# Kernel tuning notes

Measured on AMD Instinct MI355X. Metric: run time of the kernel, lower is better.

## Reference

```python
import jax, jax.numpy as jnp
import numpy as np

R_MIN = 0.01
R_MAX = 0.6
H = 32            # polar radial bins (after pooling)
W = 64            # polar angular bins (after pooling)
UP_R = 10         # radial upsampling factor
UP_T = 10         # angular upsampling factor
ATT_ALPHA = 5.0
B, C, IMG = 64, 3, 224


def _conv(x, w, b):
    # NCHW valid conv, stride 1 (matches nn.Conv2d default padding=0)
    y = jax.lax.conv_general_dilated(x, w, (1, 1), 'VALID',
                                     dimension_numbers=('NCHW', 'OIHW', 'NCHW'))
    return y + b[None, :, None, None]


def _maxpool2(x):
    return jax.lax.reduce_window(x, -jnp.inf, jax.lax.max,
                                 (1, 1, 2, 2), (1, 1, 2, 2), 'VALID')


def _grid_sample_border(x, grid):
    # F.grid_sample, bilinear, padding_mode='border', align_corners=False
    Bn, Cn, Hi, Wi = x.shape
    ix = ((grid[..., 0] + 1.0) * Wi - 1.0) * 0.5   # x-coord -> width index
    iy = ((grid[..., 1] + 1.0) * Hi - 1.0) * 0.5   # y-coord -> height index
    x0f = jnp.floor(ix)
    y0f = jnp.floor(iy)
    wx = (ix - x0f)[..., None]
    wy = (iy - y0f)[..., None]
    x0 = jnp.clip(x0f.astype(jnp.int32), 0, Wi - 1)
    x1 = jnp.clip(x0f.astype(jnp.int32) + 1, 0, Wi - 1)
    y0 = jnp.clip(y0f.astype(jnp.int32), 0, Hi - 1)
    y1 = jnp.clip(y0f.astype(jnp.int32) + 1, 0, Hi - 1)
    bidx = jnp.arange(Bn)[:, None, None]
    v00 = x[bidx, :, y0, x0]   # [B,Hg,Wg,C]
    v01 = x[bidx, :, y0, x1]
    v10 = x[bidx, :, y1, x0]
    v11 = x[bidx, :, y1, x1]
    out = (v00 * (1 - wx) * (1 - wy) + v01 * wx * (1 - wy)
           + v10 * (1 - wx) * wy + v11 * wx * wy)
    return jnp.transpose(out, (0, 3, 1, 2))  # [B,C,Hg,Wg]


def setup_inputs() -> dict:
    key = jax.random.key(0)
    ks = jax.random.split(key, 10)
    x = jax.random.normal(ks[0], (B, C, IMG, IMG), dtype=jnp.float32)
    l_t_prev = jax.random.uniform(ks[1], (B, 2), dtype=jnp.float32)
    conv1_w = jax.random.normal(ks[2], (6, C, 5, 5), dtype=jnp.float32) * 0.1
    conv1_b = jnp.zeros((6,), jnp.float32)
    conv2_w = jax.random.normal(ks[3], (16, 6, 5, 5), dtype=jnp.float32) * 0.1
    conv2_b = jnp.zeros((16,), jnp.float32)
    fc1_w = jax.random.normal(ks[4], (8, 16), dtype=jnp.float32) * 0.1
    fc1_b = jnp.zeros((8,), jnp.float32)
    fc2_w = jax.random.normal(ks[5], (2, 8), dtype=jnp.float32) * 0.1
    fc2_b = jnp.zeros((2,), jnp.float32)
    return dict(x=x, l_t_prev=l_t_prev, conv1_w=conv1_w, conv1_b=conv1_b,
                conv2_w=conv2_w, conv2_b=conv2_b, fc1_w=fc1_w, fc1_b=fc1_b,
                fc2_w=fc2_w, fc2_b=fc2_b)


def reference(x, l_t_prev, conv1_w, conv1_b, conv2_w, conv2_b,
              fc1_w, fc1_b, fc2_w, fc2_b):
    # --- attention branch: conv -> maxpool -> conv -> GAP -> fc -> sigmoid ---
    h = _conv(x, conv1_w, conv1_b)
    h = _maxpool2(h)
    h = _conv(h, conv2_w, conv2_b)
    feat = h.mean(axis=(2, 3))                     # AdaptiveAvgPool2d(1), [B,16]
    h = jax.nn.relu(feat @ fc1_w.T + fc1_b)
    weight = jax.nn.sigmoid(h @ fc2_w.T + fc2_b) * ATT_ALPHA   # [B,2]
    # --- per-batch log-polar grid ---
    Hg, Wg = H * UP_R, W * UP_T
    angle = 2.0 * jnp.pi * jnp.arange(Wg, dtype=jnp.float32) / Wg
    unit = jnp.stack([jnp.sin(angle), jnp.cos(angle)], axis=-1)   # [Wg,2]
    start = jnp.log(R_MIN * weight[:, 0])
    stop = jnp.log(R_MAX * weight[:, 1])
    t = jnp.arange(Hg, dtype=jnp.float32) / (Hg - 1)
    radii = jnp.exp(start[:, None] + (stop - start)[:, None] * t[None])  # [B,Hg]
    grid = radii[:, :, None, None] * unit[None, None]     # [B,Hg,Wg,2]
    grid = grid + l_t_prev[:, None, None, :]
    # --- irregular bilinear sampling + box filter ---
    sampled = _grid_sample_border(x, grid)                 # [B,C,Hg,Wg]
    Bn, Cn = sampled.shape[:2]
    pooled = sampled.reshape(Bn, Cn, H, UP_R, W, UP_T).mean(axis=(3, 5))
    return pooled, weight
```

## Files before the change

### kernel.cpp

```cpp
#include <hip/hip_runtime.h>
#include <math.h>

#define Bn    64
#define Cn    3
#define IMG   224
#define PLANE (IMG*IMG)
#define C1    6
#define P1    110
#define P2    106
#define NVALID (P2*P2)
#define Hh    32
#define Ww    64
#define UPR   10
#define UPT   10
#define Hg    (Hh*UPR)
#define Wg    (Ww*UPT)
#define POOLED_SIZE (Bn*Cn*Hh*Ww)
#define NCHUNK 28
#define PSTRIDE 152
#define ROWB  (IMG*8)
#define TPB1  448

typedef unsigned short u16;
typedef unsigned long long ull;
typedef _Float16 h8v __attribute__((ext_vector_type(8)));
typedef float f4v __attribute__((ext_vector_type(4)));

#define PART_FLOATS ((size_t)Bn * NCHUNK * PSTRIDE)
#define X4B_U16     ((size_t)Bn * PLANE * 4)
#define WS_NEEDED   ((PART_FLOATS + Bn * 2) * 4 + X4B_U16 * 2)

__device__ __forceinline__ unsigned hpack(float a, float b) {
    union { _Float16 h; u16 u; } x, y;
    x.h = (_Float16)a; y.h = (_Float16)b;
    return (unsigned)x.u | ((unsigned)y.u << 16);
}
__device__ __forceinline__ float h2lo(unsigned v) {
    union { _Float16 h; u16 u; } c; c.u = (u16)(v & 0xffffu); return (float)c.h;
}
__device__ __forceinline__ float h2hi(unsigned v) {
    union { _Float16 h; u16 u; } c; c.u = (u16)(v >> 16); return (float)c.h;
}

#define GSHFL(v, idx) __shfl((v), (lane & 48) + (idx), 64)

__device__ __forceinline__ void conv_chunk(
    const unsigned char* xs, const h8v* a, f4v binit,
    int wid, int lane, int n, int g, int tid, int chunk,
    float (*rowR)[C1][4], float (*edgeLo)[C1][4], float (*edgeHi)[C1][4],
    float* __restrict__ partial_slot)
{
    float colsum[4][4];
    #pragma unroll
    for (int py = 0; py < 4; ++py)
        #pragma unroll
        for (int e = 0; e < 4; ++e) colsum[py][e] = 0.0f;

    #pragma unroll
    for (int si = 0; si < 2; ++si) {
        const int s = wid * 2 + si;
        const unsigned sByte = (unsigned)(s * 128 + n * 8 + g * 16);

        f4v acc[8];
        #pragma unroll
        for (int q = 0; q < 8; ++q) acc[q] = binit;

        #pragma unroll
        for (int r = 0; r < 12; ++r) {
            h8v bf;
            const unsigned char* bp = xs + r * ROWB + sByte;
            ((ull*)&bf)[0] = *(const ull*)bp;
            ((ull*)&bf)[1] = *(const ull*)(bp + 8);
            #pragma unroll
            for (int ky = 0; ky < 5; ++ky) {
                const int q = r - ky;
                if (q >= 0 && q < 8)
                    acc[q] = __builtin_amdgcn_mfma_f32_16x16x32_f16(
                        a[ky], bf, acc[q], 0, 0, 0);
            }
        }

        #pragma unroll
        for (int py = 0; py < 4; ++py) {
            #pragma unroll
            for (int e = 0; e < 4; ++e) {
                float t = fmaxf(acc[2 * py][e], acc[2 * py + 1][e]);
                t = fmaxf(t, __shfl_xor(t, 1, 64));
                if (s == 13 && n >= 12) t = 0.0f;
                colsum[py][e] += t;
                const int oc = g * 4 + e;
                if (s == 0) {
                    const float c0 = GSHFL(t, 0), c1 = GSHFL(t, 2);
                    const float c2 = GSHFL(t, 4), c3 = GSHFL(t, 6);
                    const float S1 = c0, S2 = S1 + c1, S3 = S2 + c2, S4 = S3 + c3;
                    const float sv = (n == 0) ? S1 : (n == 1) ? S2 : (n == 2) ? S3 : S4;
                    if (n < 4 && oc < C1) edgeLo[py][oc][n] = sv;
                }
                if (s == 13) {
                    const float d109 = GSHFL(t, 10), d108 = GSHFL(t, 8);
                    const float d107 = GSHFL(t, 6),  d106 = GSHFL(t, 4);
                    const float U1 = d109, U2 = U1 + d108, U3 = U2 + d107, U4 = U3 + d106;
                    const float uv = (n == 0) ? U1 : (n == 1) ? U2 : (n == 2) ? U3 : U4;
                    if (n < 4 && oc < C1) edgeHi[py][oc][n] = uv;
                }
            }
        }
    }

    #pragma unroll
    for (int py = 0; py < 4; ++py) {
        #pragma unroll
        for (int e = 0; e < 4; ++e) {
            float v = colsum[py][e];
            v += __shfl_xor(v, 2, 64);
            v += __shfl_xor(v, 4, 64);
            v += __shfl_xor(v, 8, 64);
            const int oc = g * 4 + e;
            if (n == 0 && oc < C1) rowR[wid][oc][py] = v;
        }
    }
    __syncthreads();

    if (tid < 150) {
        const int oc = tid / 25;
        const int rem = tid - oc * 25;
        const int ky = rem / 5, kx = rem - ky * 5;
        float total = 0.0f;
        #pragma unroll
        for (int py = 0; py < 4; ++py) {
            const int y = chunk * 4 + py;
            const bool valid = (y < P1) && ((unsigned)(y - ky) <= 105u);
            float v = rowR[0][oc][py] + rowR[1][oc][py] + rowR[2][oc][py]
                    + rowR[3][oc][py] + rowR[4][oc][py] + rowR[5][oc][py]
                    + rowR[6][oc][py];
            if (kx > 0) v -= edgeLo[py][oc][kx - 1];
            if (kx < 4) v -= edgeHi[py][oc][3 - kx];
            total += valid ? v : 0.0f;
        }
        partial_slot[tid] = total;
    }
}

__global__ __launch_bounds__(TPB1) void k1_fused(
    const float* __restrict__ x,
    const float* __restrict__ w1,
    const float* __restrict__ b1,
    float* __restrict__ partial,
    u16* __restrict__ x4h,
    int do_pack)
{
    __shared__ __attribute__((aligned(16))) unsigned char xs[12 * ROWB + 128];
    __shared__ __attribute__((aligned(16))) _Float16 sa[5][64][8];
    __shared__ float rowR[7][C1][4];
    __shared__ float edgeLo[4][C1][4];
    __shared__ float edgeHi[4][C1][4];

    const int l    = blockIdx.x;
    const int b    = (l & 7) + 8 * ((l >> 3) & 7);
    const int cp   = l >> 6;
    const int chunk0 = 2 * cp, chunk1 = 2 * cp + 1;
    const int gy00 = chunk0 * 8, gy01 = chunk1 * 8;
    const int tid  = threadIdx.x;
    const int wid  = tid >> 6;
    const int lane = tid & 63;
    const int n    = lane & 15;
    const int g    = lane >> 4;

    const float* xb = x + (size_t)b * (Cn * PLANE);
    u16* ob = x4h + (size_t)b * PLANE * 4;

    if (wid == 0) {
        #pragma unroll
        for (int ky = 0; ky < 5; ++ky) {
            #pragma unroll
            for (int j = 0; j < 8; ++j) {
                const int kmem = g * 8 + j;
                const int ic = kmem & 3, kx = kmem >> 2;
                float w = 0.0f;
                if (n < C1 && ic < 3 && kx < 5)
                    w = w1[((n * 3 + ic) * 5 + ky) * 5 + kx];
                sa[ky][lane][j] = (_Float16)w;
            }
        }
    } else {
        for (int i = tid - 64; i < 12 * 112; i += TPB1 - 64) {
            const int r = i / 112;
            const int p = i - r * 112;
            const int gy = gy00 + r;
            uint4 U; U.x = U.y = U.z = U.w = 0u;
            if (gy < IMG) {
                const float2 v0 = *(const float2*)(xb + 0 * PLANE + gy * IMG + 2 * p);
                const float2 v1 = *(const float2*)(xb + 1 * PLANE + gy * IMG + 2 * p);
                const float2 v2 = *(const float2*)(xb + 2 * PLANE + gy * IMG + 2 * p);
                U.x = hpack(v0.x, v1.x);
                U.y = hpack(v2.x, 0.0f);
                U.z = hpack(v0.y, v1.y);
                U.w = hpack(v2.y, 0.0f);
            }
            *(uint4*)(xs + r * ROWB + p * 16) = U;
            if (do_pack && r < 8)
                *(uint4*)(ob + ((size_t)gy * IMG + 2 * p) * 4) = U;
        }
    }
    __syncthreads();

    h8v a[5];
    #pragma unroll
    for (int ky = 0; ky < 5; ++ky) a[ky] = *(const h8v*)&sa[ky][lane][0];
    f4v binit;
    #pragma unroll
    for (int e = 0; e < 4; ++e) {
        const int oc = g * 4 + e;
        binit[e] = (oc < C1) ? b1[oc] : 0.0f;
    }

    float2 rv0[3], rv1[3], rv2[3];
    #pragma unroll
    for (int k = 0; k < 3; ++k) {
        const int i = tid + k * TPB1;
        const int r = i / 112, p = i - r * 112;
        const int gy = gy01 + r;
        float2 z; z.x = 0.0f; z.y = 0.0f;
        rv0[k] = z; rv1[k] = z; rv2[k] = z;
        if (gy < IMG) {
            rv0[k] = *(const float2*)(xb + 0 * PLANE + gy * IMG + 2 * p);
            rv1[k] = *(const float2*)(xb + 1 * PLANE + gy * IMG + 2 * p);
            rv2[k] = *(const float2*)(xb + 2 * PLANE + gy * IMG + 2 * p);
        }
    }

    conv_chunk(xs, a, binit, wid, lane, n, g, tid, chunk0,
               rowR, edgeLo, edgeHi,
               partial + ((size_t)b * NCHUNK + chunk0) * PSTRIDE);
    __syncthreads();

    #pragma unroll
    for (int k = 0; k < 3; ++k) {
        const int i = tid + k * TPB1;
        const int r = i / 112, p = i - r * 112;
        uint4 U;
        U.x = hpack(rv0[k].x, rv1[k].x);
        U.y = hpack(rv2[k].x, 0.0f);
        U.z = hpack(rv0[k].y, rv1[k].y);
        U.w = hpack(rv2[k].y, 0.0f);
        *(uint4*)(xs + r * ROWB + p * 16) = U;
        const int gy = gy01 + r;
        if (do_pack && r < 8 && gy < IMG)
            *(uint4*)(ob + ((size_t)gy * IMG + 2 * p) * 4) = U;
    }
    __syncthreads();

    conv_chunk(xs, a, binit, wid, lane, n, g, tid, chunk1,
               rowR, edgeLo, edgeHi,
               partial + ((size_t)b * NCHUNK + chunk1) * PSTRIDE);
}

__global__ __launch_bounds__(256) void k2_head(
    const float* __restrict__ partial, const float* __restrict__ w2,
    const float* __restrict__ b2, const float* __restrict__ fc1w,
    const float* __restrict__ fc1b, const float* __restrict__ fc2w,
    const float* __restrict__ fc2b, float* __restrict__ wt_ws,
    float* __restrict__ out)
{
    const int b = blockIdx.x;
    const int tid = threadIdx.x;
    __shared__ float wsb[150];
    __shared__ float sfeat[16];
    __shared__ float sh[8];

    if (tid < 150) {
        const float* p = partial + (size_t)b * NCHUNK * PSTRIDE + tid;
        float s = 0.0f;
        #pragma unroll
        for (int c = 0; c < NCHUNK; ++c) s += p[c * PSTRIDE];
        wsb[tid] = s;
    }
    __syncthreads();
    if (tid < 16) {
        float s = 0.0f;
        for (int j = 0; j < 150; ++j) s += w2[tid * 150 + j] * wsb[j];
        sfeat[tid] = b2[tid] + s * (1.0f / (float)NVALID);
    }
    __syncthreads();
    if (tid < 8) {
        float s = fc1b[tid];
        #pragma unroll
        for (int j = 0; j < 16; ++j) s += fc1w[tid * 16 + j] * sfeat[j];
        sh[tid] = fmaxf(s, 0.0f);
    }
    __syncthreads();
    if (tid < 2) {
        float s = fc2b[tid];
        #pragma unroll
        for (int j = 0; j < 8; ++j) s += fc2w[tid * 8 + j] * sh[j];
        float sig = (s >= 0.0f) ? (1.0f / (1.0f + expf(-s)))
                                : (expf(s) / (1.0f + expf(s)));
        const float wgt = 5.0f * sig;
        wt_ws[b * 2 + tid] = wgt;
        out[POOLED_SIZE + b * 2 + tid] = wgt;
    }
}

__device__ __forceinline__ void sample_coords(
    float gxn, float gyn, int& x0, int& y0, float& wx, float& wy)
{
    float ix = ((gxn + 1.0f) * (float)IMG - 1.0f) * 0.5f;
    float iy = ((gyn + 1.0f) * (float)IMG - 1.0f) * 0.5f;
    ix = fminf(fmaxf(ix, 0.0f), (float)(IMG - 1));
    iy = fminf(fmaxf(iy, 0.0f), (float)(IMG - 1));
    x0 = (int)ix; if (x0 > IMG - 2) x0 = IMG - 2;
    y0 = (int)iy; if (y0 > IMG - 2) y0 = IMG - 2;
    wx = ix - (float)x0;
    wy = iy - (float)y0;
}

__global__ __launch_bounds__(640) void k3_sample_pool_f16(
    const u16* __restrict__ x4h,
    const float* __restrict__ ltp,
    const float* __restrict__ wt,
    float* __restrict__ out)
{
    __shared__ float part[3 * Wg];

    const int L = blockIdx.x;
    const int q = L >> 3;
    const int h = q & 31;
    const int b = (L & 7) + 8 * (q >> 5);
    const int tid = threadIdx.x;

    const float w0 = wt[b * 2 + 0];
    const float w1 = wt[b * 2 + 1];
    const float l0 = ltp[b * 2 + 0];
    const float l1 = ltp[b * 2 + 1];
    const float start = logf(0.01f * w0);
    const float stop  = logf(0.6f  * w1);
    const float dr = stop - start;

    const float angle = 6.283185307179586f * (float)tid / (float)Wg;
    const float sn = __sinf(angle);
    const float cs = __cosf(angle);

    const u16* xb4 = x4h + (size_t)b * PLANE * 4;

    const float ratio = expf(dr * (1.0f / (float)(Hg - 1)));
    float r = expf(start + dr * ((float)(h * UPR) / (float)(Hg - 1)));

    float acc0 = 0.0f, acc1 = 0.0f, acc2 = 0.0f;
    #pragma unroll
    for (int i = 0; i < UPR; ++i) {
        int x0, y0; float wx, wy;
        sample_coords(r * sn + l0, r * cs + l1, x0, y0, wx, wy);
        r *= ratio;

        const u16* base = xb4 + ((size_t)(y0 * IMG + x0)) * 4;
        const uint4 R0 = *(const uint4*)(base);
        const uint4 R1 = *(const uint4*)(base + IMG * 4);

        const float wx0 = 1.0f - wx, wy0 = 1.0f - wy;
        const float w00 = wx0 * wy0, w01 = wx * wy0;
        const float w10 = wx0 * wy,  w11 = wx * wy;

        acc0 += w00*h2lo(R0.x) + w01*h2lo(R0.z) + w10*h2lo(R1.x) + w11*h2lo(R1.z);
        acc1 += w00*h2hi(R0.x) + w01*h2hi(R0.z) + w10*h2hi(R1.x) + w11*h2hi(R1.z);
        acc2 += w00*h2lo(R0.y) + w01*h2lo(R0.w) + w10*h2lo(R1.y) + w11*h2lo(R1.w);
    }
    part[0 * Wg + tid] = acc0;
    part[1 * Wg + tid] = acc1;
    part[2 * Wg + tid] = acc2;
    __syncthreads();

    if (tid < Cn * Ww) {
        const int c = tid / Ww;
        const int w = tid % Ww;
        const float* p = part + c * Wg + w * UPT;
        float s = 0.0f;
        #pragma unroll
        for (int j = 0; j < UPT; ++j) s += p[j];
        out[(((size_t)b * Cn + c) * Hh + h) * Ww + w] = s * (1.0f / (UPR * UPT));
    }
}

__global__ __launch_bounds__(640) void k3_sample_pool_nchw(
    const float* __restrict__ x, const float* __restrict__ ltp,
    const float* __restrict__ wt, float* __restrict__ out)
{
    __shared__ float part[3 * Wg];
    const int L = blockIdx.x;
    const int q = L >> 3;
    const int h = q & 31;
    const int b = (L & 7) + 8 * (q >> 5);
    const int tid = threadIdx.x;

    const float w0 = wt[b * 2 + 0];
    const float w1 = wt[b * 2 + 1];
    const float l0 = ltp[b * 2 + 0];
    const float l1 = ltp[b * 2 + 1];
    const float start = logf(0.01f * w0);
    const float stop  = logf(0.6f  * w1);
    const float dr = stop - start;
    const float angle = 6.283185307179586f * (float)tid / (float)Wg;
    const float sn = __sinf(angle);
    const float cs = __cosf(angle);
    const float* xb = x + (size_t)b * Cn * PLANE;

    const float ratio = expf(dr * (1.0f / (float)(Hg - 1)));
    float r = expf(start + dr * ((float)(h * UPR) / (float)(Hg - 1)));

    float acc0 = 0.0f, acc1 = 0.0f, acc2 = 0.0f;
    #pragma unroll
    for (int i = 0; i < UPR; ++i) {
        int x0, y0; float wx, wy;
        sample_coords(r * sn + l0, r * cs + l1, x0, y0, wx, wy);
        r *= ratio;
        const float wx0 = 1.0f - wx, wy0 = 1.0f - wy;
        const float w00 = wx0 * wy0, w01 = wx * wy0;
        const float w10 = wx0 * wy,  w11 = wx * wy;
        const int o00 = y0 * IMG + x0;
        acc0 += w00*xb[o00] + w01*xb[o00+1] + w10*xb[o00+IMG] + w11*xb[o00+IMG+1];
        const float* x1p = xb + PLANE;
        acc1 += w00*x1p[o00] + w01*x1p[o00+1] + w10*x1p[o00+IMG] + w11*x1p[o00+IMG+1];
        const float* x2p = xb + 2 * PLANE;
        acc2 += w00*x2p[o00] + w01*x2p[o00+1] + w10*x2p[o00+IMG] + w11*x2p[o00+IMG+1];
    }
    part[0 * Wg + tid] = acc0;
    part[1 * Wg + tid] = acc1;
    part[2 * Wg + tid] = acc2;
    __syncthreads();

    if (tid < Cn * Ww) {
        const int c = tid / Ww;
        const int w = tid % Ww;
        const float* p = part + c * Wg + w * UPT;
        float s = 0.0f;
        #pragma unroll
        for (int j = 0; j < UPT; ++j) s += p[j];
        out[(((size_t)b * Cn + c) * Hh + h) * Ww + w] = s * (1.0f / (UPR * UPT));
    }
}

extern "C" void kernel_launch(void* const* d_in, const int* in_sizes, int n_in,
                              void* d_out, int out_size, void* d_ws, size_t ws_size,
                              hipStream_t stream) {
    const float* x       = (const float*)d_in[0];
    const float* ltp     = (const float*)d_in[1];
    const float* conv1_w = (const float*)d_in[2];
    const float* conv1_b = (const float*)d_in[3];
    const float* conv2_w = (const float*)d_in[4];
    const float* conv2_b = (const float*)d_in[5];
    const float* fc1_w   = (const float*)d_in[6];
    const float* fc1_b   = (const float*)d_in[7];
    const float* fc2_w   = (const float*)d_in[8];
    const float* fc2_b   = (const float*)d_in[9];
    float* out = (float*)d_out;

    const int do_pack = (ws_size >= WS_NEEDED) ? 1 : 0;

    float* part_ws = (float*)d_ws;
    float* wt_ws   = part_ws + PART_FLOATS;
    u16*   x4h     = (u16*)(wt_ws + Bn * 2);

    k1_fused<<<dim3(Bn * NCHUNK / 2), dim3(TPB1), 0, stream>>>(
        x, conv1_w, conv1_b, part_ws, x4h, do_pack);
    k2_head<<<dim3(Bn), dim3(256), 0, stream>>>(part_ws, conv2_w, conv2_b,
                                                fc1_w, fc1_b, fc2_w, fc2_b,
                                                wt_ws, out);
    if (do_pack)
        k3_sample_pool_f16<<<dim3(Hh * Bn), dim3(Wg), 0, stream>>>(x4h, ltp, wt_ws, out);
    else
        k3_sample_pool_nchw<<<dim3(Hh * Bn), dim3(Wg), 0, stream>>>(x, ltp, wt_ws, out);
}
```

Measured before the change: 179.0 us.

## Split conv blocks to one chunk each and batch sampler gather loads

```diff
diff --git a/kernel.cpp b/kernel.cpp
--- a/kernel.cpp
+++ b/kernel.cpp
@@ -7,8 +7,7 @@
 #define PLANE (IMG*IMG)
 #define C1    6
 #define P1    110
-#define P2    106
-#define NVALID (P2*P2)
+#define NVALID (106*106)
 #define Hh    32
 #define Ww    64
 #define UPR   10
@@ -44,12 +43,77 @@
 
 #define GSHFL(v, idx) __shfl((v), (lane & 48) + (idx), 64)
 
-__device__ __forceinline__ void conv_chunk(
-    const unsigned char* xs, const h8v* a, f4v binit,
-    int wid, int lane, int n, int g, int tid, int chunk,
-    float (*rowR)[C1][4], float (*edgeLo)[C1][4], float (*edgeHi)[C1][4],
-    float* __restrict__ partial_slot)
+__global__ __launch_bounds__(TPB1) void k1_fused(
+    const float* __restrict__ x,
+    const float* __restrict__ w1,
+    const float* __restrict__ b1,
+    float* __restrict__ partial,
+    u16* __restrict__ x4h,
+    int do_pack)
 {
+    __shared__ __attribute__((aligned(16))) unsigned char xs[12 * ROWB + 128];
+    __shared__ __attribute__((aligned(16))) _Float16 sa[5][64][8];
+    __shared__ float rowR[7][C1][4];
+    __shared__ float edgeLo[4][C1][4];
+    __shared__ float edgeHi[4][C1][4];
+
+    const int b     = blockIdx.x;
+    const int chunk = blockIdx.y;
+    const int tid   = threadIdx.x;
+    const int wid   = tid >> 6;
+    const int lane  = tid & 63;
+    const int n     = lane & 15;
+    const int g     = lane >> 4;
+    const int gy0   = chunk * 8;
+
+    const float* xb = x + (size_t)b * (Cn * PLANE);
+    u16* ob = x4h + (size_t)b * PLANE * 4;
+
+    if (wid == 0) {
+        #pragma unroll
+        for (int ky = 0; ky < 5; ++ky) {
+            #pragma unroll
+            for (int j = 0; j < 8; ++j) {
+                const int kmem = g * 8 + j;
+                const int ic = kmem & 3, kx = kmem >> 2;
+                float w = 0.0f;
+                if (n < C1 && ic < 3 && kx < 5)
+                    w = w1[((n * 3 + ic) * 5 + ky) * 5 + kx];
+                sa[ky][lane][j] = (_Float16)w;
+            }
+        }
+    } else {
+        for (int i = tid - 64; i < 12 * 112; i += TPB1 - 64) {
+            const int r = i / 112;
+            const int p = i - r * 112;
+            const int gy = gy0 + r;
+            uint4 U; U.x = U.y = U.z = U.w = 0u;
+            if (gy < IMG) {
+                const float2 v0 = *(const float2*)(xb + 0 * PLANE + gy * IMG + 2 * p);
+                const float2 v1 = *(const float2*)(xb + 1 * PLANE + gy * IMG + 2 * p);
+                const float2 v2 = *(const float2*)(xb + 2 * PLANE + gy * IMG + 2 * p);
+                U.x = hpack(v0.x, v1.x);
+                U.y = hpack(v2.x, 0.0f);
+                U.z = hpack(v0.y, v1.y);
+                U.w = hpack(v2.y, 0.0f);
+            }
+            *(uint4*)(xs + r * ROWB + p * 16) = U;
+            if (do_pack && r < 8)
+                *(uint4*)(ob + ((size_t)gy * IMG + 2 * p) * 4) = U;
+        }
+    }
+    __syncthreads();
+
+    h8v a[5];
+    #pragma unroll
+    for (int ky = 0; ky < 5; ++ky) a[ky] = *(const h8v*)&sa[ky][lane][0];
+    f4v binit;
+    #pragma unroll
+    for (int e = 0; e < 4; ++e) {
+        const int oc = g * 4 + e;
+        binit[e] = (oc < C1) ? b1[oc] : 0.0f;
+    }
+
     float colsum[4][4];
     #pragma unroll
     for (int py = 0; py < 4; ++py)
@@ -137,122 +201,8 @@
             if (kx < 4) v -= edgeHi[py][oc][3 - kx];
             total += valid ? v : 0.0f;
         }
-        partial_slot[tid] = total;
-    }
-}
-
-__global__ __launch_bounds__(TPB1) void k1_fused(
-    const float* __restrict__ x,
-    const float* __restrict__ w1,
-    const float* __restrict__ b1,
-    float* __restrict__ partial,
-    u16* __restrict__ x4h,
-    int do_pack)
-{
-    __shared__ __attribute__((aligned(16))) unsigned char xs[12 * ROWB + 128];
-    __shared__ __attribute__((aligned(16))) _Float16 sa[5][64][8];
-    __shared__ float rowR[7][C1][4];
-    __shared__ float edgeLo[4][C1][4];
-    __shared__ float edgeHi[4][C1][4];
-
-    const int l    = blockIdx.x;
-    const int b    = (l & 7) + 8 * ((l >> 3) & 7);
-    const int cp   = l >> 6;
-    const int chunk0 = 2 * cp, chunk1 = 2 * cp + 1;
-    const int gy00 = chunk0 * 8, gy01 = chunk1 * 8;
-    const int tid  = threadIdx.x;
-    const int wid  = tid >> 6;
-    const int lane = tid & 63;
-    const int n    = lane & 15;
-    const int g    = lane >> 4;
-
-    const float* xb = x + (size_t)b * (Cn * PLANE);
-    u16* ob = x4h + (size_t)b * PLANE * 4;
-
-    if (wid == 0) {
-        #pragma unroll
-        for (int ky = 0; ky < 5; ++ky) {
-            #pragma unroll
-            for (int j = 0; j < 8; ++j) {
-                const int kmem = g * 8 + j;
-                const int ic = kmem & 3, kx = kmem >> 2;
-                float w = 0.0f;
-                if (n < C1 && ic < 3 && kx < 5)
-                    w = w1[((n * 3 + ic) * 5 + ky) * 5 + kx];
-                sa[ky][lane][j] = (_Float16)w;
-            }
-        }
-    } else {
-        for (int i = tid - 64; i < 12 * 112; i += TPB1 - 64) {
-            const int r = i / 112;
-            const int p = i - r * 112;
-            const int gy = gy00 + r;
-            uint4 U; U.x = U.y = U.z = U.w = 0u;
-            if (gy < IMG) {
-                const float2 v0 = *(const float2*)(xb + 0 * PLANE + gy * IMG + 2 * p);
-                const float2 v1 = *(const float2*)(xb + 1 * PLANE + gy * IMG + 2 * p);
-                const float2 v2 = *(const float2*)(xb + 2 * PLANE + gy * IMG + 2 * p);
-                U.x = hpack(v0.x, v1.x);
-                U.y = hpack(v2.x, 0.0f);
-                U.z = hpack(v0.y, v1.y);
-                U.w = hpack(v2.y, 0.0f);
-            }
-            *(uint4*)(xs + r * ROWB + p * 16) = U;
-            if (do_pack && r < 8)
-                *(uint4*)(ob + ((size_t)gy * IMG + 2 * p) * 4) = U;
-        }
-    }
-    __syncthreads();
-
-    h8v a[5];
-    #pragma unroll
-    for (int ky = 0; ky < 5; ++ky) a[ky] = *(const h8v*)&sa[ky][lane][0];
-    f4v binit;
-    #pragma unroll
-    for (int e = 0; e < 4; ++e) {
-        const int oc = g * 4 + e;
-        binit[e] = (oc < C1) ? b1[oc] : 0.0f;
-    }
-
-    float2 rv0[3], rv1[3], rv2[3];
-    #pragma unroll
-    for (int k = 0; k < 3; ++k) {
-        const int i = tid + k * TPB1;
-        const int r = i / 112, p = i - r * 112;
-        const int gy = gy01 + r;
-        float2 z; z.x = 0.0f; z.y = 0.0f;
-        rv0[k] = z; rv1[k] = z; rv2[k] = z;
-        if (gy < IMG) {
-            rv0[k] = *(const float2*)(xb + 0 * PLANE + gy * IMG + 2 * p);
-            rv1[k] = *(const float2*)(xb + 1 * PLANE + gy * IMG + 2 * p);
-            rv2[k] = *(const float2*)(xb + 2 * PLANE + gy * IMG + 2 * p);
-        }
-    }
-
-    conv_chunk(xs, a, binit, wid, lane, n, g, tid, chunk0,
-               rowR, edgeLo, edgeHi,
-               partial + ((size_t)b * NCHUNK + chunk0) * PSTRIDE);
-    __syncthreads();
-
-    #pragma unroll
-    for (int k = 0; k < 3; ++k) {
-        const int i = tid + k * TPB1;
-        const int r = i / 112, p = i - r * 112;
-        uint4 U;
-        U.x = hpack(rv0[k].x, rv1[k].x);
-        U.y = hpack(rv2[k].x, 0.0f);
-        U.z = hpack(rv0[k].y, rv1[k].y);
-        U.w = hpack(rv2[k].y, 0.0f);
-        *(uint4*)(xs + r * ROWB + p * 16) = U;
-        const int gy = gy01 + r;
-        if (do_pack && r < 8 && gy < IMG)
-            *(uint4*)(ob + ((size_t)gy * IMG + 2 * p) * 4) = U;
-    }
-    __syncthreads();
-
-    conv_chunk(xs, a, binit, wid, lane, n, g, tid, chunk1,
-               rowR, edgeLo, edgeHi,
-               partial + ((size_t)b * NCHUNK + chunk1) * PSTRIDE);
+        partial[((size_t)b * NCHUNK + chunk) * PSTRIDE + tid] = total;
+    }
 }
 
 __global__ __launch_bounds__(256) void k2_head(
@@ -342,27 +292,40 @@
 
     const u16* xb4 = x4h + (size_t)b * PLANE * 4;
 
-    const float ratio = expf(dr * (1.0f / (float)(Hg - 1)));
-    float r = expf(start + dr * ((float)(h * UPR) / (float)(Hg - 1)));
+    int xi[UPR], yi[UPR];
+    float wxa[UPR], wya[UPR];
+    #pragma unroll
+    for (int i = 0; i < UPR; ++i) {
+        const float ri = __expf(start + dr * ((float)(h * UPR + i)
+                                              * (1.0f / (float)(Hg - 1))));
+        sample_coords(ri * sn + l0, ri * cs + l1, xi[i], yi[i], wxa[i], wya[i]);
+    }
 
     float acc0 = 0.0f, acc1 = 0.0f, acc2 = 0.0f;
     #pragma unroll
-    for (int i = 0; i < UPR; ++i) {
-        int x0, y0; float wx, wy;
-        sample_coords(r * sn + l0, r * cs + l1, x0, y0, wx, wy);
-        r *= ratio;
-
-        const u16* base = xb4 + ((size_t)(y0 * IMG + x0)) * 4;
-        const uint4 R0 = *(const uint4*)(base);
-        const uint4 R1 = *(const uint4*)(base + IMG * 4);
-
-        const float wx0 = 1.0f - wx, wy0 = 1.0f - wy;
-        const float w00 = wx0 * wy0, w01 = wx * wy0;
-        const float w10 = wx0 * wy,  w11 = wx * wy;
-
-        acc0 += w00*h2lo(R0.x) + w01*h2lo(R0.z) + w10*h2lo(R1.x) + w11*h2lo(R1.z);
-        acc1 += w00*h2hi(R0.x) + w01*h2hi(R0.z) + w10*h2hi(R1.x) + w11*h2hi(R1.z);
-        acc2 += w00*h2lo(R0.y) + w01*h2lo(R0.w) + w10*h2lo(R1.y) + w11*h2lo(R1.w);
+    for (int bb = 0; bb < 2; ++bb) {
+        uint4 R0[5], R1[5];
+        #pragma unroll
+        for (int i = 0; i < 5; ++i) {
+            const int s = bb * 5 + i;
+            const u16* base = xb4 + ((size_t)(yi[s] * IMG + xi[s])) * 4;
+            R0[i] = *(const uint4*)(base);
+            R1[i] = *(const uint4*)(base + IMG * 4);
+        }
+        #pragma unroll
+        for (int i = 0; i < 5; ++i) {
+            const int s = bb * 5 + i;
+            const float wx = wxa[s], wy = wya[s];
+            const float wx0 = 1.0f - wx, wy0 = 1.0f - wy;
+            const float w00 = wx0 * wy0, w01 = wx * wy0;
+            const float w10 = wx0 * wy,  w11 = wx * wy;
+            acc0 += w00*h2lo(R0[i].x) + w01*h2lo(R0[i].z)
+                  + w10*h2lo(R1[i].x) + w11*h2lo(R1[i].z);
+            acc1 += w00*h2hi(R0[i].x) + w01*h2hi(R0[i].z)
+                  + w10*h2hi(R1[i].x) + w11*h2hi(R1[i].z);
+            acc2 += w00*h2lo(R0[i].y) + w01*h2lo(R0[i].w)
+                  + w10*h2lo(R1[i].y) + w11*h2lo(R1[i].w);
+        }
     }
     part[0 * Wg + tid] = acc0;
     part[1 * Wg + tid] = acc1;
@@ -403,15 +366,13 @@
     const float cs = __cosf(angle);
     const float* xb = x + (size_t)b * Cn * PLANE;
 
-    const float ratio = expf(dr * (1.0f / (float)(Hg - 1)));
-    float r = expf(start + dr * ((float)(h * UPR) / (float)(Hg - 1)));
-
     float acc0 = 0.0f, acc1 = 0.0f, acc2 = 0.0f;
     #pragma unroll
     for (int i = 0; i < UPR; ++i) {
+        const float ri = __expf(start + dr * ((float)(h * UPR + i)
+                                              * (1.0f / (float)(Hg - 1))));
         int x0, y0; float wx, wy;
-        sample_coords(r * sn + l0, r * cs + l1, x0, y0, wx, wy);
-        r *= ratio;
+        sample_coords(ri * sn + l0, ri * cs + l1, x0, y0, wx, wy);
         const float wx0 = 1.0f - wx, wy0 = 1.0f - wy;
         const float w00 = wx0 * wy0, w01 = wx * wy0;
         const float w10 = wx0 * wy,  w11 = wx * wy;
@@ -459,7 +420,7 @@
     float* wt_ws   = part_ws + PART_FLOATS;
     u16*   x4h     = (u16*)(wt_ws + Bn * 2);
 
-    k1_fused<<<dim3(Bn * NCHUNK / 2), dim3(TPB1), 0, stream>>>(
+    k1_fused<<<dim3(Bn, NCHUNK), dim3(TPB1), 0, stream>>>(
         x, conv1_w, conv1_b, part_ws, x4h, do_pack);
     k2_head<<<dim3(Bn), dim3(256), 0, stream>>>(part_ws, conv2_w, conv2_b,
                                                 fc1_w, fc1_b, fc2_w, fc2_b,
```

After: 173.3 us. -3.2%, faster.
